# Optimization experiments

Measured on AMD Instinct MI355X. Metric: run time of the kernel, lower is better.

The kernel has to match this reference:

```python
import jax, jax.numpy as jnp
import numpy as np

P, D = 8192, 512


def setup_inputs() -> dict:
    key = jax.random.key(0)
    ks = jax.random.split(key, 8)
    s = 1.0 / np.sqrt(D)
    return {
        "F_chunks": jax.random.normal(ks[0], (P, D), dtype=jnp.float32),
        "Wq": jax.random.normal(ks[1], (D, D), dtype=jnp.float32) * s,
        "bq": jax.random.normal(ks[2], (D,), dtype=jnp.float32) * 0.01,
        "Wk": jax.random.normal(ks[3], (D, D), dtype=jnp.float32) * s,
        "bk": jax.random.normal(ks[4], (D,), dtype=jnp.float32) * 0.01,
        "Wv": jax.random.normal(ks[5], (D, D), dtype=jnp.float32) * s,
        "bv": jax.random.normal(ks[6], (D,), dtype=jnp.float32) * 0.01,
        "lam": jnp.float32(2.0),
    }


def _cdist_l2(x):
    # pairwise Euclidean distance, grad-safe at zero (matches torch.cdist values)
    sq_norm = jnp.sum(x * x, axis=-1)                       # [p]
    sq = sq_norm[:, None] + sq_norm[None, :] - 2.0 * (x @ x.T)  # [p, p]
    sq = jnp.maximum(sq, 0.0)
    safe = jnp.where(sq > 0.0, sq, 1.0)
    return jnp.where(sq > 0.0, jnp.sqrt(safe), 0.0)


def reference(F_chunks, Wq, bq, Wk, bk, Wv, bv, lam):
    p, d = F_chunks.shape
    Q = F_chunks @ Wq.T + bq
    K = F_chunks @ Wk.T + bk
    V = F_chunks @ Wv.T + bv
    logits = (Q @ K.T) * (1.0 / np.sqrt(d))                 # [p, p]
    dist = _cdist_l2(F_chunks)                               # [p, p]
    attn = jax.nn.softmax(logits - lam * dist, axis=-1)      # [p, p]
    F_out = attn @ V                                         # [p, d]
    return (F_out, dist)
```

## Files before the change

kernel.cpp:

```cpp
#include <hip/hip_runtime.h>

#define PP 8192
#define DD 512
#define NJT (PP / 64)
#define NSPLIT 2
#define NJT3 (PP / NSPLIT / 32)

typedef short bf16x8 __attribute__((ext_vector_type(8)));
typedef float f32x4 __attribute__((ext_vector_type(4)));
typedef unsigned short u16;
typedef unsigned int u32;

__device__ __forceinline__ u16 f2bf(float x) {
  u32 u = __float_as_uint(x);
  u += 0x7fffu + ((u >> 16) & 1u);
  return (u16)(u >> 16);
}
__device__ __forceinline__ float bf2f(u16 h) {
  return __uint_as_float(((u32)h) << 16);
}
__device__ __forceinline__ f32x4 mfma_bf16(bf16x8 a, bf16x8 b, f32x4 c) {
  return __builtin_amdgcn_mfma_f32_16x16x32_bf16(a, b, c, 0, 0, 0);
}
__device__ __forceinline__ void gload_lds16(const u16* g, u16* l) {
  __builtin_amdgcn_global_load_lds(
      (const __attribute__((address_space(1))) void*)g,
      (__attribute__((address_space(3))) void*)l, 16, 0, 0);
}

__global__ void prep_wt_kernel(const float* __restrict__ Wq, const float* __restrict__ Wk,
                               const float* __restrict__ Wv, u16* __restrict__ WqT,
                               u16* __restrict__ WkT, u16* __restrict__ Wvb) {
  int i = blockIdx.x * 256 + threadIdx.x;
  int a = i >> 9, k = i & 511;
  WqT[(size_t)k * DD + a] = f2bf(Wq[i]);
  WkT[(size_t)k * DD + a] = f2bf(Wk[i]);
  Wvb[i] = f2bf(Wv[i]);
}

__global__ void kb_kernel(const float* __restrict__ Wk, const float* __restrict__ bq,
                          float* __restrict__ kb) {
  int k = threadIdx.x;
  float s = 0.f;
  for (int a = 0; a < DD; ++a) s += bq[a] * Wk[(size_t)a * DD + k];
  kb[k] = s * 0.04419417382415922f;
}

__global__ void prep_f_kernel(const float* __restrict__ F, const float* __restrict__ kb,
                              u16* __restrict__ Fb, float2* __restrict__ nv) {
  int wid = threadIdx.x >> 6, lane = threadIdx.x & 63;
  int row = blockIdx.x * 4 + wid;
  const float* src = F + (size_t)row * DD + lane * 8;
  float4 a = *(const float4*)src;
  float4 b = *(const float4*)(src + 4);
  float v[8] = {a.x, a.y, a.z, a.w, b.x, b.y, b.z, b.w};
  const float* kp = kb + lane * 8;
  float4 ka = *(const float4*)kp;
  float4 kc = *(const float4*)(kp + 4);
  float kw[8] = {ka.x, ka.y, ka.z, ka.w, kc.x, kc.y, kc.z, kc.w};
  u16 h[8];
  float s = 0.f, d = 0.f;
#pragma unroll
  for (int j = 0; j < 8; ++j) {
    h[j] = f2bf(v[j]);
    float f = bf2f(h[j]);
    s += f * f;
    d += f * kw[j];
  }
  u32 pk[4];
#pragma unroll
  for (int j = 0; j < 4; ++j) pk[j] = (u32)h[2 * j] | ((u32)h[2 * j + 1] << 16);
  *(uint4*)(Fb + (size_t)row * DD + lane * 8) = make_uint4(pk[0], pk[1], pk[2], pk[3]);
#pragma unroll
  for (int dd = 1; dd < 64; dd <<= 1) { s += __shfl_xor(s, dd); d += __shfl_xor(d, dd); }
  if (lane == 0) nv[row] = make_float2(s, d);
}

__global__ __launch_bounds__(256) void mt_kernel(const u16* __restrict__ WkT,
                                                 const u16* __restrict__ WqT,
                                                 u16* __restrict__ MT) {
  int lane = threadIdx.x & 63, wm = threadIdx.x >> 6;
  int l15 = lane & 15, lg = lane >> 4;
  int rowA = blockIdx.x * 64 + wm * 16 + l15;
  int rowC0 = blockIdx.x * 64 + wm * 16 + lg * 4;
  int colbase = blockIdx.y * 64;
  f32x4 z = {0.f, 0.f, 0.f, 0.f};
  f32x4 acc[4] = {z, z, z, z};
#pragma unroll
  for (int kk = 0; kk < 16; ++kk) {
    bf16x8 aF = *(const bf16x8*)(WkT + (size_t)rowA * DD + kk * 32 + lg * 8);
#pragma unroll
    for (int nf = 0; nf < 4; ++nf) {
      bf16x8 bW = *(const bf16x8*)(WqT + (size_t)(colbase + nf * 16 + l15) * DD + kk * 32 + lg * 8);
      acc[nf] = mfma_bf16(aF, bW, acc[nf]);
    }
  }
  const float isd = 0.04419417382415922f;
#pragma unroll
  for (int nf = 0; nf < 4; ++nf) {
    int col = colbase + nf * 16 + l15;
#pragma unroll
    for (int r = 0; r < 4; ++r)
      MT[(size_t)(rowC0 + r) * DD + col] = f2bf(acc[nf][r] * isd);
  }
}

__global__ __launch_bounds__(256) void gv_kernel(
    const u16* __restrict__ Fb, const u16* __restrict__ MT, const u16* __restrict__ Wvb,
    const float* __restrict__ bv, u16* __restrict__ G, u16* __restrict__ Vt) {
  int mat = blockIdx.z;
  const u16* W = (mat == 0) ? MT : Wvb;
  int lane = threadIdx.x & 63, wm = threadIdx.x >> 6;
  int l15 = lane & 15, lg = lane >> 4;
  int rowA = blockIdx.x * 64 + wm * 16 + l15;
  int rowC0 = blockIdx.x * 64 + wm * 16 + lg * 4;
  int colbase = blockIdx.y * 64;
  f32x4 z = {0.f, 0.f, 0.f, 0.f};
  f32x4 acc[4] = {z, z, z, z};
#pragma unroll
  for (int kk = 0; kk < 16; ++kk) {
    bf16x8 aF = *(const bf16x8*)(Fb + (size_t)rowA * DD + kk * 32 + lg * 8);
#pragma unroll
    for (int nf = 0; nf < 4; ++nf) {
      bf16x8 bW = *(const bf16x8*)(W + (size_t)(colbase + nf * 16 + l15) * DD + kk * 32 + lg * 8);
      acc[nf] = mfma_bf16(aF, bW, acc[nf]);
    }
  }
#pragma unroll
  for (int nf = 0; nf < 4; ++nf) {
    int col = colbase + nf * 16 + l15;
    if (mat == 1) {
      float bb = bv[col];
      ushort4 vv = make_ushort4(f2bf(acc[nf][0] + bb), f2bf(acc[nf][1] + bb),
                                f2bf(acc[nf][2] + bb), f2bf(acc[nf][3] + bb));
      *(ushort4*)(Vt + (size_t)col * PP + rowC0) = vv;
    } else {
#pragma unroll
      for (int r = 0; r < 4; ++r)
        G[(size_t)(rowC0 + r) * DD + col] = f2bf(acc[nf][r]);
    }
  }
}

__global__ __launch_bounds__(256)
__attribute__((amdgpu_waves_per_eu(2, 4))) void sd3_kernel(
    const u16* __restrict__ G, const u16* __restrict__ Fb,
    const float2* __restrict__ nv, const float* __restrict__ lamp,
    float* __restrict__ Dist, u16* __restrict__ P, float* __restrict__ partial) {
  const float lam = lamp[0];
  int lane = threadIdx.x & 63, wid = threadIdx.x >> 6;
  int wm = wid >> 1, wn = wid & 1;
  int l15 = lane & 15, lg = lane >> 4;
  int rowA = blockIdx.x * 32 + wm * 16 + l15;
  int rowC0 = blockIdx.x * 32 + wm * 16 + lg * 4;
  int kbase = blockIdx.y * (PP / NSPLIT);

  __shared__ u16 Ftile[2][32][DD];

  bf16x8 gf[16], ff[16];
#pragma unroll
  for (int c = 0; c < 16; ++c) {
    gf[c] = *(const bf16x8*)(G + (size_t)rowA * DD + c * 32 + lg * 8);
    ff[c] = *(const bf16x8*)(Fb + (size_t)rowA * DD + c * 32 + lg * 8);
  }
  float ni[4];
#pragma unroll
  for (int r = 0; r < 4; ++r) ni[r] = nv[rowC0 + r].x;
  float rs[4] = {0.f, 0.f, 0.f, 0.f};
  f32x4 z = {0.f, 0.f, 0.f, 0.f};

  int kl = wn * 16 + l15;
  int swz = kl & 7;

#pragma unroll
  for (int t = 0; t < 8; ++t) {
    int row = wid * 8 + t;
    gload_lds16(Fb + (size_t)(kbase + row) * DD + ((lane ^ (row & 7)) * 8),
                &Ftile[0][row][0]);
  }
  __syncthreads();

#pragma unroll 1
  for (int jt = 0; jt < NJT3; ++jt) {
    int key0 = kbase + jt * 32;
    int cur = jt & 1;
    if (jt + 1 < NJT3) {
#pragma unroll
      for (int t = 0; t < 8; ++t) {
        int row = wid * 8 + t;
        gload_lds16(Fb + (size_t)(key0 + 32 + row) * DD + ((lane ^ (row & 7)) * 8),
                    &Ftile[cur ^ 1][row][0]);
      }
    }
    const u16* ft = &Ftile[cur][0][0];
    f32x4 sqk0 = z, sqk1 = z, sff0 = z, sff1 = z;
#pragma unroll
    for (int kk = 0; kk < 16; kk += 2) {
      bf16x8 bF0 = *(const bf16x8*)(ft + (size_t)kl * DD + (((kk * 4 + lg) ^ swz) * 8));
      bf16x8 bF1 = *(const bf16x8*)(ft + (size_t)kl * DD + ((((kk + 1) * 4 + lg) ^ swz) * 8));
      sqk0 = mfma_bf16(gf[kk], bF0, sqk0);
      sff0 = mfma_bf16(ff[kk], bF0, sff0);
      sqk1 = mfma_bf16(gf[kk + 1], bF1, sqk1);
      sff1 = mfma_bf16(ff[kk + 1], bF1, sff1);
    }
    int colB = key0 + kl;
    float2 nvj = nv[colB];
#pragma unroll
    for (int r = 0; r < 4; ++r) {
      float sq = ni[r] + nvj.x - 2.0f * (sff0[r] + sff1[r]);
      sq = fmaxf(sq, 0.f);
      float dist = sqrtf(sq);
      Dist[(size_t)(rowC0 + r) * PP + colB] = dist;
      float s = (sqk0[r] + sqk1[r]) + nvj.y - lam * dist;
      float p = __expf(fminf(s, 60.f));
      P[(size_t)(rowC0 + r) * PP + colB] = f2bf(p);
      rs[r] += p;
    }
    __syncthreads();
  }
#pragma unroll
  for (int d = 1; d < 16; d <<= 1) {
#pragma unroll
    for (int r = 0; r < 4; ++r) rs[r] += __shfl_xor(rs[r], d);
  }
  if (l15 == 0) {
#pragma unroll
    for (int r = 0; r < 4; ++r)
      partial[(size_t)(blockIdx.y * 2 + wn) * PP + rowC0 + r] = rs[r];
  }
}

__global__ void rowsum_kernel(const float* __restrict__ partial, float* __restrict__ rowsum) {
  int r = blockIdx.x * 256 + threadIdx.x;
  float s = 0.f;
#pragma unroll
  for (int cb = 0; cb < 4; ++cb) s += partial[(size_t)cb * PP + r];
  rowsum[r] = s;
}

#define KB 256
__global__ __launch_bounds__(256) void pv2_kernel(
    const u16* __restrict__ P, const u16* __restrict__ Vt,
    const float* __restrict__ rowsum, float* __restrict__ Fout) {
  int lane = threadIdx.x & 63, wid = threadIdx.x >> 6;
  int l15 = lane & 15, lg = lane >> 4;
  int q0 = blockIdx.x * 64;
  int col0 = blockIdx.y * 128 + wid * 32;
  __shared__ u16 Pt[2][64][KB];
  f32x4 z = {0.f, 0.f, 0.f, 0.f};
  f32x4 o[4][2] = {{z, z}, {z, z}, {z, z}, {z, z}};

#pragma unroll
  for (int i = 0; i < 8; ++i) {
    int row = wid * 16 + i * 2 + (lane >> 5);
    int g = (lane & 24) | ((lane & 7) ^ (row & 7));
    gload_lds16(P + (size_t)(q0 + row) * PP + g * 8, &Pt[0][wid * 16 + i * 2][0]);
  }
  __syncthreads();

#pragma unroll 1
  for (int kt = 0; kt < PP / KB; ++kt) {
    int cur = kt & 1;
    if (kt + 1 < PP / KB) {
      int k0n = (kt + 1) * KB;
#pragma unroll
      for (int i = 0; i < 8; ++i) {
        int row = wid * 16 + i * 2 + (lane >> 5);
        int g = (lane & 24) | ((lane & 7) ^ (row & 7));
        gload_lds16(P + (size_t)(q0 + row) * PP + k0n + g * 8,
                    &Pt[cur ^ 1][wid * 16 + i * 2][0]);
      }
    }
    int k0 = kt * KB;
#pragma unroll
    for (int kc = 0; kc < KB / 32; ++kc) {
      bf16x8 aP[4];
#pragma unroll
      for (int qf = 0; qf < 4; ++qf) {
        int row = qf * 16 + l15;
        int cg = kc * 4 + lg;
        int gp = (cg & 24) | ((cg & 7) ^ (row & 7));
        aP[qf] = *(const bf16x8*)(&Pt[cur][row][0] + gp * 8);
      }
#pragma unroll
      for (int nt = 0; nt < 2; ++nt) {
        int n = col0 + nt * 16 + l15;
        bf16x8 bV = *(const bf16x8*)(Vt + (size_t)n * PP + k0 + kc * 32 + lg * 8);
#pragma unroll
        for (int qf = 0; qf < 4; ++qf) o[qf][nt] = mfma_bf16(aP[qf], bV, o[qf][nt]);
      }
    }
    __syncthreads();
  }
  float inv[4][4];
#pragma unroll
  for (int qf = 0; qf < 4; ++qf)
#pragma unroll
    for (int r = 0; r < 4; ++r)
      inv[qf][r] = 1.0f / rowsum[q0 + qf * 16 + lg * 4 + r];
#pragma unroll
  for (int qf = 0; qf < 4; ++qf) {
#pragma unroll
    for (int nt = 0; nt < 2; ++nt) {
#pragma unroll
      for (int r = 0; r < 4; ++r)
        Fout[(size_t)(q0 + qf * 16 + lg * 4 + r) * DD + col0 + nt * 16 + l15] =
            o[qf][nt][r] * inv[qf][r];
    }
  }
}

__global__ __launch_bounds__(512)
__attribute__((amdgpu_waves_per_eu(2, 2))) void fused_kernel(
    const u16* __restrict__ G, const u16* __restrict__ Fb, const u16* __restrict__ Vt,
    const float2* __restrict__ nv, const float* __restrict__ lamp,
    float* __restrict__ out) {
  float* Fout = out;
  float* Dist = out + (size_t)PP * DD;
  const float lam = lamp[0];
  int lane = threadIdx.x & 63, wid = threadIdx.x >> 6;
  int wm = wid >> 2, wn = wid & 3;
  int l15 = lane & 15, lg = lane >> 4;
  int rowA = blockIdx.x * 32 + wm * 16 + l15;
  int rowC0 = blockIdx.x * 32 + wm * 16 + lg * 4;

  __shared__ u16 Ftile[2][64][DD];
  __shared__ u16 P_lds[32][72];
  __shared__ float redmax[8][16];
  __shared__ float redsum[8][16];

  bf16x8 gf[16], ff[16];
#pragma unroll
  for (int c = 0; c < 16; ++c) {
    gf[c] = *(const bf16x8*)(G + (size_t)rowA * DD + c * 32 + lg * 8);
    ff[c] = *(const bf16x8*)(Fb + (size_t)rowA * DD + c * 32 + lg * 8);
  }
  float ni[4];
#pragma unroll
  for (int r = 0; r < 4; ++r) ni[r] = nv[rowC0 + r].x;
  float m_run[2][4], l_run[2][4];
#pragma unroll
  for (int g = 0; g < 2; ++g)
#pragma unroll
    for (int r = 0; r < 4; ++r) { m_run[g][r] = -1e30f; l_run[g][r] = 0.f; }
  f32x4 z = {0.f, 0.f, 0.f, 0.f};
  f32x4 o[8] = {z, z, z, z, z, z, z, z};

  int kl = wn * 16 + l15;
  int swz = kl & 7;
  int col0 = wid * 64;

#pragma unroll
  for (int t = 0; t < 8; ++t) {
    int row = wid * 8 + t;
    gload_lds16(Fb + (size_t)row * DD + ((lane ^ (row & 7)) * 8), &Ftile[0][row][0]);
  }
  __syncthreads();

#pragma unroll 1
  for (int jt = 0; jt < NJT; ++jt) {
    int key0 = jt * 64;
    int cur = jt & 1;
    if (jt + 1 < NJT) {
      int nb = cur ^ 1;
#pragma unroll
      for (int t = 0; t < 8; ++t) {
        int row = wid * 8 + t;
        gload_lds16(Fb + (size_t)(key0 + 64 + row) * DD + ((lane ^ (row & 7)) * 8),
                    &Ftile[nb][row][0]);
      }
    }
    const u16* ft = &Ftile[cur][0][0];
    f32x4 sqk = z, sff = z;
#pragma unroll
    for (int kk = 0; kk < 16; ++kk) {
      bf16x8 bF = *(const bf16x8*)(ft + (size_t)kl * DD + (((kk * 4 + lg) ^ swz) * 8));
      sqk = mfma_bf16(gf[kk], bF, sqk);
      sff = mfma_bf16(ff[kk], bF, sff);
    }
    int colB = key0 + kl;
    float2 nvj = nv[colB];
    float pv[4], tmax[4];
#pragma unroll
    for (int r = 0; r < 4; ++r) {
      float sq = ni[r] + nvj.x - 2.0f * sff[r];
      sq = fmaxf(sq, 0.f);
      float dist = sqrtf(sq);
      Dist[(size_t)(rowC0 + r) * PP + colB] = dist;
      float s = sqk[r] + nvj.y - lam * dist;
      pv[r] = s;
      tmax[r] = s;
    }
#pragma unroll
    for (int d = 1; d < 16; d <<= 1) {
#pragma unroll
      for (int r = 0; r < 4; ++r) tmax[r] = fmaxf(tmax[r], __shfl_xor(tmax[r], d));
    }
    if (l15 == 0) {
#pragma unroll
      for (int r = 0; r < 4; ++r) redmax[wid][lg * 4 + r] = tmax[r];
    }
    __syncthreads();
    float mnew[2][4], alpha[2][4];
#pragma unroll
    for (int g = 0; g < 2; ++g) {
#pragma unroll
      for (int r = 0; r < 4; ++r) {
        float mt = m_run[g][r];
#pragma unroll
        for (int ow = 0; ow < 4; ++ow) mt = fmaxf(mt, redmax[g * 4 + ow][lg * 4 + r]);
        mnew[g][r] = mt;
        alpha[g][r] = __expf(m_run[g][r] - mt);
      }
    }
    float tsum[4];
#pragma unroll
    for (int r = 0; r < 4; ++r) {
      float mo = (wm == 0) ? mnew[0][r] : mnew[1][r];
      pv[r] = __expf(pv[r] - mo);
      tsum[r] = pv[r];
    }
#pragma unroll
    for (int d = 1; d < 16; d <<= 1) {
#pragma unroll
      for (int r = 0; r < 4; ++r) tsum[r] += __shfl_xor(tsum[r], d);
    }
#pragma unroll
    for (int r = 0; r < 4; ++r)
      P_lds[wm * 16 + lg * 4 + r][wn * 16 + l15] = f2bf(pv[r]);
    if (l15 == 0) {
#pragma unroll
      for (int r = 0; r < 4; ++r) redsum[wid][lg * 4 + r] = tsum[r];
    }
    __syncthreads();
#pragma unroll
    for (int g = 0; g < 2; ++g) {
#pragma unroll
      for (int r = 0; r < 4; ++r) {
        float s4 = 0.f;
#pragma unroll
        for (int ow = 0; ow < 4; ++ow) s4 += redsum[g * 4 + ow][lg * 4 + r];
        l_run[g][r] = l_run[g][r] * alpha[g][r] + s4;
        m_run[g][r] = mnew[g][r];
      }
    }
#pragma unroll
    for (int g = 0; g < 2; ++g) {
#pragma unroll
      for (int nt = 0; nt < 4; ++nt) {
#pragma unroll
        for (int r = 0; r < 4; ++r) o[g * 4 + nt][r] *= alpha[g][r];
      }
    }
#pragma unroll
    for (int kc = 0; kc < 2; ++kc) {
      bf16x8 aP0 = *(const bf16x8*)(&P_lds[l15][kc * 32 + lg * 8]);
      bf16x8 aP1 = *(const bf16x8*)(&P_lds[16 + l15][kc * 32 + lg * 8]);
#pragma unroll
      for (int nt = 0; nt < 4; ++nt) {
        int n = col0 + nt * 16 + l15;
        bf16x8 bV = *(const bf16x8*)(Vt + (size_t)n * PP + key0 + kc * 32 + lg * 8);
        o[nt] = mfma_bf16(aP0, bV, o[nt]);
        o[4 + nt] = mfma_bf16(aP1, bV, o[4 + nt]);
      }
    }
  }
  float inv[2][4];
#pragma unroll
  for (int g = 0; g < 2; ++g)
#pragma unroll
    for (int r = 0; r < 4; ++r) inv[g][r] = 1.0f / l_run[g][r];
#pragma unroll
  for (int g = 0; g < 2; ++g) {
#pragma unroll
    for (int nt = 0; nt < 4; ++nt) {
#pragma unroll
      for (int r = 0; r < 4; ++r)
        Fout[(size_t)(blockIdx.x * 32 + g * 16 + lg * 4 + r) * DD + col0 + nt * 16 + l15] =
            o[g * 4 + nt][r] * inv[g][r];
    }
  }
}

extern "C" void kernel_launch(void* const* d_in, const int* in_sizes, int n_in,
                              void* d_out, int out_size, void* d_ws, size_t ws_size,
                              hipStream_t stream) {
  const float* F   = (const float*)d_in[0];
  const float* Wq  = (const float*)d_in[1];
  const float* bq  = (const float*)d_in[2];
  const float* Wk  = (const float*)d_in[3];
  const float* bk  = (const float*)d_in[4];
  const float* Wv  = (const float*)d_in[5];
  const float* bv  = (const float*)d_in[6];
  const float* lam = (const float*)d_in[7];
  float* out = (float*)d_out;
  (void)bk;

  u16* ws  = (u16*)d_ws;
  u16* Fb  = ws;
  u16* G   = Fb + (size_t)PP * DD;
  u16* Vt  = G + (size_t)PP * DD;
  u16* WqT = Vt + (size_t)PP * DD;
  u16* WkT = WqT + (size_t)DD * DD;
  u16* Wvb = WkT + (size_t)DD * DD;
  u16* MT  = Wvb + (size_t)DD * DD;
  float2* nv = (float2*)(MT + (size_t)DD * DD);
  float* kb  = (float*)(nv + PP);
  u16* P        = (u16*)(kb + DD);
  float* partial = (float*)(P + (size_t)PP * PP);
  float* rowsum  = partial + (size_t)4 * PP;
  size_t need = (size_t)((char*)(rowsum + PP) - (char*)d_ws);

  prep_wt_kernel<<<1024, 256, 0, stream>>>(Wq, Wk, Wv, WqT, WkT, Wvb);
  kb_kernel<<<1, 512, 0, stream>>>(Wk, bq, kb);
  prep_f_kernel<<<PP / 4, 256, 0, stream>>>(F, kb, Fb, nv);
  mt_kernel<<<dim3(8, 8), 256, 0, stream>>>(WkT, WqT, MT);
  gv_kernel<<<dim3(PP / 64, DD / 64, 2), 256, 0, stream>>>(Fb, MT, Wvb, bv, G, Vt);

  if (ws_size >= need) {
    float* Dist = out + (size_t)PP * DD;
    sd3_kernel<<<dim3(PP / 32, NSPLIT), 256, 0, stream>>>(G, Fb, nv, lam, Dist, P, partial);
    rowsum_kernel<<<PP / 256, 256, 0, stream>>>(partial, rowsum);
    pv2_kernel<<<dim3(PP / 64, 4), 256, 0, stream>>>(P, Vt, rowsum, out);
  } else {
    fused_kernel<<<PP / 32, 512, 0, stream>>>(G, Fb, Vt, nv, lam, out);
  }
}
```

Baseline: 507.2 us.

## Parallelize kb reduction, use fast sqrt, and software-prefetch operands in PV kernel

Three separate changes. The key-bias kernel now runs as 16 blocks that split the reduction across warps and combine the partials in shared memory, instead of a single block with a 512-long serial loop per thread. The distance computation switches to the hardware sqrt builtin. The PV kernel loads the next k-chunk's P fragments from LDS and V fragments from global into registers before issuing the current chunk's MFMAs, so load latency can overlap compute at the cost of extra registers.

Result: faster. 473.6 us, median of 2 (-6.6%).

```diff
diff --git a/kernel.cpp b/kernel.cpp
--- a/kernel.cpp
+++ b/kernel.cpp
@@ -40,10 +40,19 @@
 
 __global__ void kb_kernel(const float* __restrict__ Wk, const float* __restrict__ bq,
                           float* __restrict__ kb) {
-  int k = threadIdx.x;
+  __shared__ float red[8][32];
+  int kloc = threadIdx.x & 31, ag = threadIdx.x >> 5;
+  int k = blockIdx.x * 32 + kloc;
   float s = 0.f;
-  for (int a = 0; a < DD; ++a) s += bq[a] * Wk[(size_t)a * DD + k];
-  kb[k] = s * 0.04419417382415922f;
+  for (int a = ag * 64; a < ag * 64 + 64; ++a) s += bq[a] * Wk[(size_t)a * DD + k];
+  red[ag][kloc] = s;
+  __syncthreads();
+  if (threadIdx.x < 32) {
+    float t = 0.f;
+#pragma unroll
+    for (int g = 0; g < 8; ++g) t += red[g][threadIdx.x];
+    kb[blockIdx.x * 32 + threadIdx.x] = t * 0.04419417382415922f;
+  }
 }
 
 __global__ void prep_f_kernel(const float* __restrict__ F, const float* __restrict__ kb,
@@ -209,7 +218,7 @@
     for (int r = 0; r < 4; ++r) {
       float sq = ni[r] + nvj.x - 2.0f * (sff0[r] + sff1[r]);
       sq = fmaxf(sq, 0.f);
-      float dist = sqrtf(sq);
+      float dist = __builtin_amdgcn_sqrtf(sq);
       Dist[(size_t)(rowC0 + r) * PP + colB] = dist;
       float s = (sqk0[r] + sqk1[r]) + nvj.y - lam * dist;
       float p = __expf(fminf(s, 60.f));
@@ -261,6 +270,19 @@
 #pragma unroll 1
   for (int kt = 0; kt < PP / KB; ++kt) {
     int cur = kt & 1;
+    int k0 = kt * KB;
+    bf16x8 aPc[4], bVc[2];
+#pragma unroll
+    for (int qf = 0; qf < 4; ++qf) {
+      int row = qf * 16 + l15;
+      int gp = ((0 * 4 + lg) & 24) | (((0 * 4 + lg) & 7) ^ (row & 7));
+      aPc[qf] = *(const bf16x8*)(&Pt[cur][row][0] + gp * 8);
+    }
+#pragma unroll
+    for (int nt = 0; nt < 2; ++nt) {
+      int n = col0 + nt * 16 + l15;
+      bVc[nt] = *(const bf16x8*)(Vt + (size_t)n * PP + k0 + lg * 8);
+    }
     if (kt + 1 < PP / KB) {
       int k0n = (kt + 1) * KB;
 #pragma unroll
@@ -271,23 +293,33 @@
                     &Pt[cur ^ 1][wid * 16 + i * 2][0]);
       }
     }
-    int k0 = kt * KB;
 #pragma unroll
     for (int kc = 0; kc < KB / 32; ++kc) {
-      bf16x8 aP[4];
-#pragma unroll
-      for (int qf = 0; qf < 4; ++qf) {
-        int row = qf * 16 + l15;
-        int cg = kc * 4 + lg;
-        int gp = (cg & 24) | ((cg & 7) ^ (row & 7));
-        aP[qf] = *(const bf16x8*)(&Pt[cur][row][0] + gp * 8);
+      bf16x8 aPn[4], bVn[2];
+      if (kc + 1 < KB / 32) {
+        int cgn = (kc + 1) * 4 + lg;
+#pragma unroll
+        for (int qf = 0; qf < 4; ++qf) {
+          int row = qf * 16 + l15;
+          int gp = (cgn & 24) | ((cgn & 7) ^ (row & 7));
+          aPn[qf] = *(const bf16x8*)(&Pt[cur][row][0] + gp * 8);
+        }
+#pragma unroll
+        for (int nt = 0; nt < 2; ++nt) {
+          int n = col0 + nt * 16 + l15;
+          bVn[nt] = *(const bf16x8*)(Vt + (size_t)n * PP + k0 + (kc + 1) * 32 + lg * 8);
+        }
       }
 #pragma unroll
       for (int nt = 0; nt < 2; ++nt) {
-        int n = col0 + nt * 16 + l15;
-        bf16x8 bV = *(const bf16x8*)(Vt + (size_t)n * PP + k0 + kc * 32 + lg * 8);
-#pragma unroll
-        for (int qf = 0; qf < 4; ++qf) o[qf][nt] = mfma_bf16(aP[qf], bV, o[qf][nt]);
+#pragma unroll
+        for (int qf = 0; qf < 4; ++qf) o[qf][nt] = mfma_bf16(aPc[qf], bVc[nt], o[qf][nt]);
+      }
+      if (kc + 1 < KB / 32) {
+#pragma unroll
+        for (int qf = 0; qf < 4; ++qf) aPc[qf] = aPn[qf];
+        bVc[0] = bVn[0];
+        bVc[1] = bVn[1];
       }
     }
     __syncthreads();
@@ -512,7 +544,7 @@
   size_t need = (size_t)((char*)(rowsum + PP) - (char*)d_ws);
 
   prep_wt_kernel<<<1024, 256, 0, stream>>>(Wq, Wk, Wv, WqT, WkT, Wvb);
-  kb_kernel<<<1, 512, 0, stream>>>(Wk, bq, kb);
+  kb_kernel<<<16, 256, 0, stream>>>(Wk, bq, kb);
   prep_f_kernel<<<PP / 4, 256, 0, stream>>>(F, kb, Fb, nv);
   mt_kernel<<<dim3(8, 8), 256, 0, stream>>>(WkT, WqT, MT);
   gv_kernel<<<dim3(PP / 64, DD / 64, 2), 256, 0, stream>>>(Fb, MT, Wvb, bv, G, Vt);
```

## Parallelize bias-key kernel, use fast sqrt, load P directly in PV

Applied to the files above, without the earlier changes.

The kb reduction now runs across 16 blocks of 256 threads with an LDS tree combine, where before it was a single block with one serial 512-long loop per thread. The distance sqrt uses the raw hardware sqrt builtin instead of the IEEE-accurate sqrtf. The PV kernel no longer stages P tiles in LDS through double-buffered async loads and reads P fragments straight from global memory in a simple unrolled loop. That removes LDS traffic and barriers, but it depends on L2/cache behaviour for the P reuse that the four column blocks used to get through shared memory.

Result: slower. 658.9 us (+29.9%).

```diff
diff --git a/kernel.cpp b/kernel.cpp
--- a/kernel.cpp
+++ b/kernel.cpp
@@ -40,10 +40,19 @@
 
 __global__ void kb_kernel(const float* __restrict__ Wk, const float* __restrict__ bq,
                           float* __restrict__ kb) {
-  int k = threadIdx.x;
+  __shared__ float red[8][32];
+  int kloc = threadIdx.x & 31, ag = threadIdx.x >> 5;
+  int k = blockIdx.x * 32 + kloc;
   float s = 0.f;
-  for (int a = 0; a < DD; ++a) s += bq[a] * Wk[(size_t)a * DD + k];
-  kb[k] = s * 0.04419417382415922f;
+  for (int a = ag * 64; a < ag * 64 + 64; ++a) s += bq[a] * Wk[(size_t)a * DD + k];
+  red[ag][kloc] = s;
+  __syncthreads();
+  if (threadIdx.x < 32) {
+    float t = 0.f;
+#pragma unroll
+    for (int g = 0; g < 8; ++g) t += red[g][threadIdx.x];
+    kb[blockIdx.x * 32 + threadIdx.x] = t * 0.04419417382415922f;
+  }
 }
 
 __global__ void prep_f_kernel(const float* __restrict__ F, const float* __restrict__ kb,
@@ -209,7 +218,7 @@
     for (int r = 0; r < 4; ++r) {
       float sq = ni[r] + nvj.x - 2.0f * (sff0[r] + sff1[r]);
       sq = fmaxf(sq, 0.f);
-      float dist = sqrtf(sq);
+      float dist = __builtin_amdgcn_sqrtf(sq);
       Dist[(size_t)(rowC0 + r) * PP + colB] = dist;
       float s = (sqk0[r] + sqk1[r]) + nvj.y - lam * dist;
       float p = __expf(fminf(s, 60.f));
@@ -238,59 +247,36 @@
   rowsum[r] = s;
 }
 
-#define KB 256
-__global__ __launch_bounds__(256) void pv2_kernel(
+__global__ __launch_bounds__(256) void pv3_kernel(
     const u16* __restrict__ P, const u16* __restrict__ Vt,
     const float* __restrict__ rowsum, float* __restrict__ Fout) {
   int lane = threadIdx.x & 63, wid = threadIdx.x >> 6;
   int l15 = lane & 15, lg = lane >> 4;
   int q0 = blockIdx.x * 64;
   int col0 = blockIdx.y * 128 + wid * 32;
-  __shared__ u16 Pt[2][64][KB];
   f32x4 z = {0.f, 0.f, 0.f, 0.f};
   f32x4 o[4][2] = {{z, z}, {z, z}, {z, z}, {z, z}};
 
-#pragma unroll
-  for (int i = 0; i < 8; ++i) {
-    int row = wid * 16 + i * 2 + (lane >> 5);
-    int g = (lane & 24) | ((lane & 7) ^ (row & 7));
-    gload_lds16(P + (size_t)(q0 + row) * PP + g * 8, &Pt[0][wid * 16 + i * 2][0]);
-  }
-  __syncthreads();
-
-#pragma unroll 1
-  for (int kt = 0; kt < PP / KB; ++kt) {
-    int cur = kt & 1;
-    if (kt + 1 < PP / KB) {
-      int k0n = (kt + 1) * KB;
-#pragma unroll
-      for (int i = 0; i < 8; ++i) {
-        int row = wid * 16 + i * 2 + (lane >> 5);
-        int g = (lane & 24) | ((lane & 7) ^ (row & 7));
-        gload_lds16(P + (size_t)(q0 + row) * PP + k0n + g * 8,
-                    &Pt[cur ^ 1][wid * 16 + i * 2][0]);
-      }
-    }
-    int k0 = kt * KB;
-#pragma unroll
-    for (int kc = 0; kc < KB / 32; ++kc) {
-      bf16x8 aP[4];
-#pragma unroll
-      for (int qf = 0; qf < 4; ++qf) {
-        int row = qf * 16 + l15;
-        int cg = kc * 4 + lg;
-        int gp = (cg & 24) | ((cg & 7) ^ (row & 7));
-        aP[qf] = *(const bf16x8*)(&Pt[cur][row][0] + gp * 8);
-      }
-#pragma unroll
-      for (int nt = 0; nt < 2; ++nt) {
-        int n = col0 + nt * 16 + l15;
-        bf16x8 bV = *(const bf16x8*)(Vt + (size_t)n * PP + k0 + kc * 32 + lg * 8);
-#pragma unroll
-        for (int qf = 0; qf < 4; ++qf) o[qf][nt] = mfma_bf16(aP[qf], bV, o[qf][nt]);
-      }
-    }
-    __syncthreads();
+  const u16* pbase[4];
+#pragma unroll
+  for (int qf = 0; qf < 4; ++qf)
+    pbase[qf] = P + (size_t)(q0 + qf * 16 + l15) * PP + lg * 8;
+  const u16* vbase[2];
+#pragma unroll
+  for (int nt = 0; nt < 2; ++nt)
+    vbase[nt] = Vt + (size_t)(col0 + nt * 16 + l15) * PP + lg * 8;
+
+#pragma unroll 2
+  for (int k0 = 0; k0 < PP; k0 += 32) {
+    bf16x8 aP[4];
+#pragma unroll
+    for (int qf = 0; qf < 4; ++qf) aP[qf] = *(const bf16x8*)(pbase[qf] + k0);
+#pragma unroll
+    for (int nt = 0; nt < 2; ++nt) {
+      bf16x8 bV = *(const bf16x8*)(vbase[nt] + k0);
+#pragma unroll
+      for (int qf = 0; qf < 4; ++qf) o[qf][nt] = mfma_bf16(aP[qf], bV, o[qf][nt]);
+    }
   }
   float inv[4][4];
 #pragma unroll
@@ -512,7 +498,7 @@
   size_t need = (size_t)((char*)(rowsum + PP) - (char*)d_ws);
 
   prep_wt_kernel<<<1024, 256, 0, stream>>>(Wq, Wk, Wv, WqT, WkT, Wvb);
-  kb_kernel<<<1, 512, 0, stream>>>(Wk, bq, kb);
+  kb_kernel<<<16, 256, 0, stream>>>(Wk, bq, kb);
   prep_f_kernel<<<PP / 4, 256, 0, stream>>>(F, kb, Fb, nv);
   mt_kernel<<<dim3(8, 8), 256, 0, stream>>>(WkT, WqT, MT);
   gv_kernel<<<dim3(PP / 64, DD / 64, 2), 256, 0, stream>>>(Fb, MT, Wvb, bv, G, Vt);
@@ -521,7 +507,7 @@
     float* Dist = out + (size_t)PP * DD;
     sd3_kernel<<<dim3(PP / 32, NSPLIT), 256, 0, stream>>>(G, Fb, nv, lam, Dist, P, partial);
     rowsum_kernel<<<PP / 256, 256, 0, stream>>>(partial, rowsum);
-    pv2_kernel<<<dim3(PP / 64, 4), 256, 0, stream>>>(P, Vt, rowsum, out);
+    pv3_kernel<<<dim3(PP / 64, 4), 256, 0, stream>>>(P, Vt, rowsum, out);
   } else {
     fused_kernel<<<PP / 32, 512, 0, stream>>>(G, Fb, Vt, nv, lam, out);
   }
```
